# Performance work log

Measured on AMD Instinct MI355X. Metric: run time of the kernel, lower is better.

The kernel has to match this reference:

```python
import jax, jax.numpy as jnp
import numpy as np

CHUNK = 8192
IGNORE_INDEX = -100


def _chunked_logsumexp(hidden, weight, bias, chunk):
    """Online (flash-style) logsumexp over the vocab dim without materializing full logits."""
    V, D = weight.shape
    n_chunks = V // chunk  # V chosen divisible by chunk
    Wc = weight.reshape(n_chunks, chunk, D)
    Bc = bias.reshape(n_chunks, chunk)
    N = hidden.shape[0]

    @jax.checkpoint  # recompute chunk logits in backward, like the original CCE
    def body(carry, wb):
        m, s = carry
        w, b = wb
        logits = hidden @ w.T + b  # [N, chunk]
        cmax = jnp.max(logits, axis=-1)
        new_m = jnp.maximum(m, cmax)
        s = s * jnp.exp(m - new_m) + jnp.sum(jnp.exp(logits - new_m[:, None]), axis=-1)
        return (new_m, s), None

    init = (jnp.full((N,), -jnp.inf, jnp.float32), jnp.zeros((N,), jnp.float32))
    (m, s), _ = jax.lax.scan(body, init, (Wc, Bc))
    return m + jnp.log(s + 1e-10)


def setup_inputs() -> dict:
    key = jax.random.key(0)
    k1, k2, k3, k4 = jax.random.split(key, 4)
    N, D, V = 2048, 1024, 131072
    return {
        "hidden": jax.random.normal(k1, (N, D), dtype=jnp.float32),
        "weight": jax.random.normal(k2, (V, D), dtype=jnp.float32) * 0.02,
        "bias": jax.random.normal(k3, (V,), dtype=jnp.float32) * 0.02,
        "labels": jax.random.randint(k4, (N,), 0, V, dtype=jnp.int32),
    }


def reference(hidden, weight, bias, labels):
    valid = labels != IGNORE_INDEX
    safe_labels = jnp.where(valid, labels, 0)
    lse = _chunked_logsumexp(hidden, weight, bias, CHUNK)  # [N]
    # target logit: only gathers the label rows of weight, never full logits
    target_logit = jnp.einsum("nd,nd->n", hidden, weight[safe_labels]) + bias[safe_labels]
    ce = jnp.where(valid, lse - target_logit, 0.0)
    n_valid = jnp.maximum(jnp.sum(valid), 1).astype(jnp.float32)
    return jnp.sum(ce) / n_valid
```

## Files before the change

kernel.cpp:

```cpp
#include <hip/hip_runtime.h>

#define IGNORE_INDEX (-100)

constexpr int N_ROWS = 2048;
constexpr int D_DIM  = 1024;
constexpr int V_DIM  = 131072;
constexpr int BM = 256, BN = 256, BK = 128;
constexpr int ROW_TILES = N_ROWS / BM;
constexpr int COL_TILES = V_DIM / BN;
constexpr int NBLK = ROW_TILES * COL_TILES;
constexpr int K_TILES = D_DIM / BK;

typedef __attribute__((ext_vector_type(4))) float f32x4;
typedef __attribute__((ext_vector_type(4))) int   i32x4;
typedef __attribute__((ext_vector_type(8))) int   i32x8;

#define SCL_A 0x7F7F7F7Fu
#define SCL_B 0x79797979u

__device__ __forceinline__ unsigned int f2fp4(float f) {
  const float a = fabsf(f);
  unsigned int c = (unsigned)(a >= 0.25f) + (unsigned)(a >= 0.75f) +
                   (unsigned)(a >= 1.25f) + (unsigned)(a >= 1.75f) +
                   (unsigned)(a >= 2.5f)  + (unsigned)(a >= 3.5f) +
                   (unsigned)(a >= 5.0f);
  return c | ((__float_as_uint(f) >> 31) << 3);
}

__global__ __launch_bounds__(256)
void cvt_fp4(const float* __restrict__ src, unsigned char* __restrict__ dst,
             float prescale) {
  const size_t i = ((size_t)blockIdx.x * 256 + (size_t)threadIdx.x) * 32;
  i32x4 o;
#pragma unroll
  for (int q = 0; q < 4; ++q) {
    unsigned int wrd = 0;
#pragma unroll
    for (int e = 0; e < 8; e += 4) {
      const float4 f = *(const float4*)&src[i + q * 8 + e];
      wrd |= f2fp4(f.x * prescale) << ((e + 0) * 4);
      wrd |= f2fp4(f.y * prescale) << ((e + 1) * 4);
      wrd |= f2fp4(f.z * prescale) << ((e + 2) * 4);
      wrd |= f2fp4(f.w * prescale) << ((e + 3) * 4);
    }
    o[q] = (int)wrd;
  }
  *(i32x4*)&dst[i / 2] = o;
}

#define BAR() __builtin_amdgcn_s_barrier()
#define SP1() __builtin_amdgcn_s_setprio(1)
#define SP0() __builtin_amdgcn_s_setprio(0)
#define SCHB() __builtin_amdgcn_sched_barrier(0)
#define VM0() asm volatile("s_waitcnt vmcnt(0)" ::: "memory")

#define STAGE(gbase, ldsoff, kt, buf)                                          \
  {                                                                            \
    _Pragma("unroll") for (int j2_ = 0; j2_ < 2; ++j2_) {                      \
      const char* g_ = (gbase) + (size_t)j2_ * 65536 + (size_t)(kt) * 64;      \
      __builtin_amdgcn_global_load_lds(                                        \
          (const __attribute__((address_space(1))) unsigned int*)g_,           \
          (__attribute__((address_space(3))) unsigned int*)(smem + (ldsoff) +  \
              (buf) * 16384 + j2_ * 8192 + (tid << 4)),                        \
          16, 0, 0);                                                           \
    }                                                                          \
  }

#define READ_FRAG(ldsoff, rowbase, dst)                                        \
  {                                                                            \
    const i32x4 d_ = *(const i32x4*)(smem + (ldsoff) +                         \
                                     ((rowbase) + l15) * 64 + gcol);           \
    dst = (i32x8){d_[0], d_[1], d_[2], d_[3], 0, 0, 0, 0};                     \
  }

__global__ __launch_bounds__(512, 1)
void lse_gemm(const unsigned char* __restrict__ hf4,
              const unsigned char* __restrict__ wf4,
              const float* __restrict__ bias,
              float* __restrict__ ps) {
  __shared__ __align__(16) char smem[69632];

  const int bid = (int)blockIdx.x;
  const int logical = (bid & 7) * (NBLK / 8) + (bid >> 3);
  const int colt = logical >> 3;
  const int m0 = (logical & 7) * BM;
  const int v0 = colt * BN;

  const int tid = threadIdx.x;
  const int w = tid >> 6, lane = tid & 63;
  (void)w;
  const int wm = (tid >> 6) >> 2, wn = (tid >> 6) & 3;
  const int l15 = lane & 15, l16g = lane >> 4;
  const int gcol = (l16g ^ ((l15 >> 1) & 3)) << 4;

  const int r_ = tid >> 2, g_ = tid & 3;
  const int G_ = g_ ^ ((r_ >> 1) & 3);
  const char* habase = (const char*)hf4 + (size_t)(m0 + r_) * 512 + G_ * 16;
  const char* wbase  = (const char*)wf4 + (size_t)(v0 + r_) * 512 + G_ * 16;

  f32x4 acc[8][4];
  const f32x4 zero = {0.f, 0.f, 0.f, 0.f};
#pragma unroll
  for (int i = 0; i < 8; ++i)
#pragma unroll
    for (int j = 0; j < 4; ++j) acc[i][j] = zero;

  i32x8 ar[2], breg[4];

  STAGE(habase, 0, 0, 0);
  STAGE(wbase, 32768, 0, 0);
  SCHB();

#pragma unroll
  for (int t = 0; t < K_TILES; ++t) {
    const int buf = t & 1;
    VM0();
    BAR();
    if (t < K_TILES - 1) {
      STAGE(habase, 0, t + 1, buf ^ 1);
      STAGE(wbase, 32768, t + 1, buf ^ 1);
      SCHB();
    }
#pragma unroll
    for (int q = 0; q < 4; ++q)
      READ_FRAG(32768 + buf * 16384, wn * 64 + q * 16, breg[q]);
    READ_FRAG(buf * 16384, wm * 128, ar[0]);
#pragma unroll
    for (int f = 0; f < 8; ++f) {
      if (f < 7) READ_FRAG(buf * 16384, wm * 128 + (f + 1) * 16, ar[(f + 1) & 1]);
      SP1();
#pragma unroll
      for (int q = 0; q < 4; ++q)
        acc[f][q] = __builtin_amdgcn_mfma_scale_f32_16x16x128_f8f6f4(
            ar[f & 1], breg[q], acc[f][q], 4, 4, 0, SCL_A, 0, SCL_B);
      SP0();
    }
  }
  __syncthreads();

  float* red = (float*)smem;
  float bv[4];
#pragma unroll
  for (int q = 0; q < 4; ++q)
    bv[q] = bias[v0 + wn * 64 + q * 16 + l15];
#pragma unroll
  for (int mi = 0; mi < 8; ++mi) {
#pragma unroll
    for (int r = 0; r < 4; ++r) {
      const float v = __expf(acc[mi][0][r] + bv[0]) + __expf(acc[mi][1][r] + bv[1]) +
                      __expf(acc[mi][2][r] + bv[2]) + __expf(acc[mi][3][r] + bv[3]);
      const int row = wm * 128 + mi * 16 + l16g * 4 + r;
      red[row * 68 + wn * 16 + l15] = v;
    }
  }
  __syncthreads();
  {
    const int row = tid >> 1, h = tid & 1;
    const float* rr = &red[row * 68 + h * 32];
    f32x4 s4 = *(const f32x4*)rr;
#pragma unroll
    for (int i = 1; i < 8; ++i) s4 += *(const f32x4*)(rr + i * 4);
    float s = s4[0] + s4[1] + s4[2] + s4[3];
    s += __shfl_xor(s, 1);
    if (h == 0) ps[(size_t)(m0 + row) * COL_TILES + colt] = s;
  }
}

__global__ __launch_bounds__(256)
void row_finalize(const float* __restrict__ ps,
                  const float* __restrict__ hidden, const float* __restrict__ weight,
                  const float* __restrict__ bias, const int* __restrict__ labels,
                  float* __restrict__ ce) {
  __shared__ float ss[4], sd[4];
  const int row = blockIdx.x;
  const int t = threadIdx.x, lane = t & 63, w = t >> 6;

  float s = 0.f;
#pragma unroll
  for (int i = 0; i < COL_TILES / 256; ++i)
    s += ps[(size_t)row * COL_TILES + t + i * 256];

  const int lbl = labels[row];
  const bool valid = (lbl != IGNORE_INDEX);
  float dot = 0.f;
  if (valid) {
    const float4 h4 = *(const float4*)&hidden[(size_t)row * D_DIM + t * 4];
    const float4 w4 = *(const float4*)&weight[(size_t)lbl * D_DIM + t * 4];
    dot = h4.x * w4.x + h4.y * w4.y + h4.z * w4.z + h4.w * w4.w;
  }
#pragma unroll
  for (int msk = 1; msk < 64; msk <<= 1) {
    s += __shfl_xor(s, msk);
    dot += __shfl_xor(dot, msk);
  }
  if (lane == 0) { ss[w] = s; sd[w] = dot; }
  __syncthreads();
  if (t == 0) {
    const float S = ss[0] + ss[1] + ss[2] + ss[3];
    const float d = sd[0] + sd[1] + sd[2] + sd[3];
    ce[row] = valid ? (logf(S + 1e-10f) - (d + bias[lbl])) : 0.f;
  }
}

__global__ __launch_bounds__(256)
void final_reduce(const float* __restrict__ ce, const int* __restrict__ labels,
                  float* __restrict__ out) {
  __shared__ float ssum[4];
  __shared__ int scnt[4];
  const int t = threadIdx.x, lane = t & 63, w = t >> 6;
  float sum = 0.f; int cnt = 0;
  for (int i = t; i < N_ROWS; i += 256) {
    sum += ce[i];
    cnt += (labels[i] != IGNORE_INDEX) ? 1 : 0;
  }
#pragma unroll
  for (int msk = 1; msk < 64; msk <<= 1) {
    sum += __shfl_xor(sum, msk);
    cnt += __shfl_xor(cnt, msk);
  }
  if (lane == 0) { ssum[w] = sum; scnt[w] = cnt; }
  __syncthreads();
  if (t == 0) {
    const float S = ssum[0] + ssum[1] + ssum[2] + ssum[3];
    const int C = scnt[0] + scnt[1] + scnt[2] + scnt[3];
    out[0] = S / fmaxf((float)C, 1.f);
  }
}

extern "C" void kernel_launch(void* const* d_in, const int* in_sizes, int n_in,
                              void* d_out, int out_size, void* d_ws, size_t ws_size,
                              hipStream_t stream) {
  const float* hidden = (const float*)d_in[0];
  const float* weight = (const float*)d_in[1];
  const float* bias   = (const float*)d_in[2];
  const int*   labels = (const int*)d_in[3];
  float* out = (float*)d_out;

  const size_t WF4_B = (size_t)V_DIM * D_DIM / 2;
  const size_t HF4_B = (size_t)N_ROWS * D_DIM / 2;
  const size_t PS_B  = (size_t)N_ROWS * COL_TILES * 4;
  const size_t CE_B  = (size_t)N_ROWS * 4;
  if (ws_size < WF4_B + HF4_B + PS_B + CE_B) return;

  char* ws = (char*)d_ws;
  unsigned char* wf4 = (unsigned char*)ws;
  unsigned char* hf4 = (unsigned char*)(ws + WF4_B);
  float* ps = (float*)(ws + WF4_B + HF4_B);
  float* ce = (float*)(ws + WF4_B + HF4_B + PS_B);

  cvt_fp4<<<(int)((size_t)V_DIM * D_DIM / 8192), 256, 0, stream>>>(weight, wf4, 64.0f);
  cvt_fp4<<<(int)((size_t)N_ROWS * D_DIM / 8192), 256, 0, stream>>>(hidden, hf4, 1.0f);
  lse_gemm<<<NBLK, 512, 0, stream>>>(hf4, wf4, bias, ps);
  row_finalize<<<N_ROWS, 256, 0, stream>>>(ps, hidden, weight, bias, labels, ce);
  final_reduce<<<1, 256, 0, stream>>>(ce, labels, out);
}
```

Baseline: 312.8 us.

## Pre-shuffle FP4 operands into MFMA fragment order and load directly to registers

The FP4 conversion kernels now write hidden and weight in a fragment-major layout that matches the MFMA operand lanes, so each lane can fetch its 16-byte fragment with one coalesced global load. The GEMM drops the LDS staging, barriers and double buffering, and instead software-pipelines global loads into rotating register buffers (three A fragments, two B sets). This removes LDS traffic and per-tile synchronisation, but it depends on L2/global latency being hidden by register prefetch with only 8 waves per CU, and A fragments are now re-read from global memory by every block rather than shared through LDS.

```diff
diff --git a/kernel.cpp b/kernel.cpp
--- a/kernel.cpp
+++ b/kernel.cpp
@@ -5,11 +5,11 @@
 constexpr int N_ROWS = 2048;
 constexpr int D_DIM  = 1024;
 constexpr int V_DIM  = 131072;
-constexpr int BM = 256, BN = 256, BK = 128;
+constexpr int BM = 256, BN = 256;
 constexpr int ROW_TILES = N_ROWS / BM;
 constexpr int COL_TILES = V_DIM / BN;
 constexpr int NBLK = ROW_TILES * COL_TILES;
-constexpr int K_TILES = D_DIM / BK;
+constexpr int K_TILES = 8;
 
 typedef __attribute__((ext_vector_type(4))) float f32x4;
 typedef __attribute__((ext_vector_type(4))) int   i32x4;
@@ -27,76 +27,58 @@
   return c | ((__float_as_uint(f) >> 31) << 3);
 }
 
+template <int FRAGS>
 __global__ __launch_bounds__(256)
-void cvt_fp4(const float* __restrict__ src, unsigned char* __restrict__ dst,
-             float prescale) {
-  const size_t i = ((size_t)blockIdx.x * 256 + (size_t)threadIdx.x) * 32;
+void cvt_shuf(const float* __restrict__ src, unsigned char* __restrict__ dst,
+              float prescale) {
+  const int oid = blockIdx.x * 256 + threadIdx.x;
+  const int l = oid & 63;
+  int rest = oid >> 6;
+  const int f = rest % FRAGS; rest /= FRAGS;
+  const int t = rest & 7; rest >>= 3;
+  const int row = rest * (FRAGS * 16) + f * 16 + (l & 15);
+  const int col0 = t * 128 + (l >> 4) * 32;
+  const float* s = src + (size_t)row * D_DIM + col0;
   i32x4 o;
 #pragma unroll
-  for (int q = 0; q < 4; ++q) {
-    unsigned int wrd = 0;
+  for (int wd = 0; wd < 4; ++wd) {
+    unsigned int v = 0;
 #pragma unroll
     for (int e = 0; e < 8; e += 4) {
-      const float4 f = *(const float4*)&src[i + q * 8 + e];
-      wrd |= f2fp4(f.x * prescale) << ((e + 0) * 4);
-      wrd |= f2fp4(f.y * prescale) << ((e + 1) * 4);
-      wrd |= f2fp4(f.z * prescale) << ((e + 2) * 4);
-      wrd |= f2fp4(f.w * prescale) << ((e + 3) * 4);
-    }
-    o[q] = (int)wrd;
-  }
-  *(i32x4*)&dst[i / 2] = o;
-}
-
-#define BAR() __builtin_amdgcn_s_barrier()
-#define SP1() __builtin_amdgcn_s_setprio(1)
-#define SP0() __builtin_amdgcn_s_setprio(0)
-#define SCHB() __builtin_amdgcn_sched_barrier(0)
-#define VM0() asm volatile("s_waitcnt vmcnt(0)" ::: "memory")
-
-#define STAGE(gbase, ldsoff, kt, buf)                                          \
-  {                                                                            \
-    _Pragma("unroll") for (int j2_ = 0; j2_ < 2; ++j2_) {                      \
-      const char* g_ = (gbase) + (size_t)j2_ * 65536 + (size_t)(kt) * 64;      \
-      __builtin_amdgcn_global_load_lds(                                        \
-          (const __attribute__((address_space(1))) unsigned int*)g_,           \
-          (__attribute__((address_space(3))) unsigned int*)(smem + (ldsoff) +  \
-              (buf) * 16384 + j2_ * 8192 + (tid << 4)),                        \
-          16, 0, 0);                                                           \
-    }                                                                          \
-  }
-
-#define READ_FRAG(ldsoff, rowbase, dst)                                        \
-  {                                                                            \
-    const i32x4 d_ = *(const i32x4*)(smem + (ldsoff) +                         \
-                                     ((rowbase) + l15) * 64 + gcol);           \
-    dst = (i32x8){d_[0], d_[1], d_[2], d_[3], 0, 0, 0, 0};                     \
-  }
+      const float4 x = *(const float4*)(s + wd * 8 + e);
+      v |= f2fp4(x.x * prescale) << ((e + 0) * 4);
+      v |= f2fp4(x.y * prescale) << ((e + 1) * 4);
+      v |= f2fp4(x.z * prescale) << ((e + 2) * 4);
+      v |= f2fp4(x.w * prescale) << ((e + 3) * 4);
+    }
+    o[wd] = (int)v;
+  }
+  *(i32x4*)(dst + (size_t)oid * 16) = o;
+}
+
+#define LDF(p)                                                                 \
+  ({ const i32x4 d_ = *(const i32x4*)(p);                                      \
+     (i32x8){d_[0], d_[1], d_[2], d_[3], 0, 0, 0, 0}; })
 
 __global__ __launch_bounds__(512, 1)
-void lse_gemm(const unsigned char* __restrict__ hf4,
-              const unsigned char* __restrict__ wf4,
+void lse_gemm(const unsigned char* __restrict__ af4,
+              const unsigned char* __restrict__ bf4,
               const float* __restrict__ bias,
               float* __restrict__ ps) {
-  __shared__ __align__(16) char smem[69632];
+  __shared__ float red[256 * 68];
 
   const int bid = (int)blockIdx.x;
   const int logical = (bid & 7) * (NBLK / 8) + (bid >> 3);
-  const int colt = logical >> 3;
-  const int m0 = (logical & 7) * BM;
-  const int v0 = colt * BN;
-
-  const int tid = threadIdx.x;
-  const int w = tid >> 6, lane = tid & 63;
-  (void)w;
-  const int wm = (tid >> 6) >> 2, wn = (tid >> 6) & 3;
+  const int ct = logical >> 3;
+  const int rt = logical & 7;
+  const int m0 = rt * BM, v0 = ct * BN;
+
+  const int tid = threadIdx.x, lane = tid & 63;
+  const int wid = tid >> 6, wm = wid >> 2, wn = wid & 3;
   const int l15 = lane & 15, l16g = lane >> 4;
-  const int gcol = (l16g ^ ((l15 >> 1) & 3)) << 4;
-
-  const int r_ = tid >> 2, g_ = tid & 3;
-  const int G_ = g_ ^ ((r_ >> 1) & 3);
-  const char* habase = (const char*)hf4 + (size_t)(m0 + r_) * 512 + G_ * 16;
-  const char* wbase  = (const char*)wf4 + (size_t)(v0 + r_) * 512 + G_ * 16;
+
+  const char* ap = (const char*)af4 + ((size_t)(rt * 2 + wm) * 64) * 1024 + lane * 16;
+  const char* bp = (const char*)bf4 + ((size_t)(ct * 4 + wn) * 32) * 1024 + lane * 16;
 
   f32x4 acc[8][4];
   const f32x4 zero = {0.f, 0.f, 0.f, 0.f};
@@ -105,40 +87,31 @@
 #pragma unroll
     for (int j = 0; j < 4; ++j) acc[i][j] = zero;
 
-  i32x8 ar[2], breg[4];
-
-  STAGE(habase, 0, 0, 0);
-  STAGE(wbase, 32768, 0, 0);
-  SCHB();
+  i32x8 ar[3], br[2][4];
+
+#pragma unroll
+  for (int q = 0; q < 4; ++q) br[0][q] = LDF(bp + q * 1024);
+  ar[0] = LDF(ap);
+  ar[1] = LDF(ap + 1024);
 
 #pragma unroll
   for (int t = 0; t < K_TILES; ++t) {
-    const int buf = t & 1;
-    VM0();
-    BAR();
     if (t < K_TILES - 1) {
-      STAGE(habase, 0, t + 1, buf ^ 1);
-      STAGE(wbase, 32768, t + 1, buf ^ 1);
-      SCHB();
-    }
-#pragma unroll
-    for (int q = 0; q < 4; ++q)
-      READ_FRAG(32768 + buf * 16384, wn * 64 + q * 16, breg[q]);
-    READ_FRAG(buf * 16384, wm * 128, ar[0]);
+#pragma unroll
+      for (int q = 0; q < 4; ++q)
+        br[(t + 1) & 1][q] = LDF(bp + (size_t)((t + 1) * 4 + q) * 1024);
+    }
 #pragma unroll
     for (int f = 0; f < 8; ++f) {
-      if (f < 7) READ_FRAG(buf * 16384, wm * 128 + (f + 1) * 16, ar[(f + 1) & 1]);
-      SP1();
+      const int s = t * 8 + f;
+      if (s < 62) ar[(s + 2) % 3] = LDF(ap + (size_t)(s + 2) * 1024);
 #pragma unroll
       for (int q = 0; q < 4; ++q)
         acc[f][q] = __builtin_amdgcn_mfma_scale_f32_16x16x128_f8f6f4(
-            ar[f & 1], breg[q], acc[f][q], 4, 4, 0, SCL_A, 0, SCL_B);
-      SP0();
-    }
-  }
-  __syncthreads();
-
-  float* red = (float*)smem;
+            ar[s % 3], br[t & 1][q], acc[f][q], 4, 4, 0, SCL_A, 0, SCL_B);
+    }
+  }
+
   float bv[4];
 #pragma unroll
   for (int q = 0; q < 4; ++q)
@@ -162,7 +135,7 @@
     for (int i = 1; i < 8; ++i) s4 += *(const f32x4*)(rr + i * 4);
     float s = s4[0] + s4[1] + s4[2] + s4[3];
     s += __shfl_xor(s, 1);
-    if (h == 0) ps[(size_t)(m0 + row) * COL_TILES + colt] = s;
+    if (h == 0) ps[(size_t)(m0 + row) * COL_TILES + ct] = s;
   }
 }
 
@@ -237,20 +210,20 @@
   float* out = (float*)d_out;
 
   const size_t WF4_B = (size_t)V_DIM * D_DIM / 2;
-  const size_t HF4_B = (size_t)N_ROWS * D_DIM / 2;
+  const size_t AF4_B = (size_t)N_ROWS * D_DIM / 2;
   const size_t PS_B  = (size_t)N_ROWS * COL_TILES * 4;
   const size_t CE_B  = (size_t)N_ROWS * 4;
-  if (ws_size < WF4_B + HF4_B + PS_B + CE_B) return;
+  if (ws_size < WF4_B + AF4_B + PS_B + CE_B) return;
 
   char* ws = (char*)d_ws;
   unsigned char* wf4 = (unsigned char*)ws;
-  unsigned char* hf4 = (unsigned char*)(ws + WF4_B);
-  float* ps = (float*)(ws + WF4_B + HF4_B);
-  float* ce = (float*)(ws + WF4_B + HF4_B + PS_B);
-
-  cvt_fp4<<<(int)((size_t)V_DIM * D_DIM / 8192), 256, 0, stream>>>(weight, wf4, 64.0f);
-  cvt_fp4<<<(int)((size_t)N_ROWS * D_DIM / 8192), 256, 0, stream>>>(hidden, hf4, 1.0f);
-  lse_gemm<<<NBLK, 512, 0, stream>>>(hf4, wf4, bias, ps);
+  unsigned char* af4 = (unsigned char*)(ws + WF4_B);
+  float* ps = (float*)(ws + WF4_B + AF4_B);
+  float* ce = (float*)(ws + WF4_B + AF4_B + PS_B);
+
+  cvt_shuf<4><<<16384, 256, 0, stream>>>(weight, wf4, 64.0f);
+  cvt_shuf<8><<<256, 256, 0, stream>>>(hidden, af4, 1.0f);
+  lse_gemm<<<NBLK, 512, 0, stream>>>(af4, wf4, bias, ps);
   row_finalize<<<N_ROWS, 256, 0, stream>>>(ps, hidden, weight, bias, labels, ce);
   final_reduce<<<1, 256, 0, stream>>>(ce, labels, out);
 }
```

Measured after the change: 435.9 us. 1.39x slower.

## Fuse weight FP4 conversion into GEMM with LDS-resident weight tiles

Applied to the files above, without the earlier changes.

Drops the separate pass that converts the whole weight matrix to FP4 in global memory. Each of 256 blocks now owns four 128-column vocab tiles and keeps the FP4 weight tile resident in LDS, double buffered. While it loops over all row tiles of the hidden states, it converts the next weight tile from fp32, interleaved with the MFMA work. This removes the global write and re-read of the FP4 weights. In exchange each block streams the hidden FP4 data once per vocab tile, uses more LDS, and the grid is only 256 blocks.

```diff
diff --git a/kernel.cpp b/kernel.cpp
--- a/kernel.cpp
+++ b/kernel.cpp
@@ -5,11 +5,11 @@
 constexpr int N_ROWS = 2048;
 constexpr int D_DIM  = 1024;
 constexpr int V_DIM  = 131072;
-constexpr int BM = 256, BN = 256, BK = 128;
+constexpr int BM = 256, BN = 128, BK = 128;
 constexpr int ROW_TILES = N_ROWS / BM;
 constexpr int COL_TILES = V_DIM / BN;
-constexpr int NBLK = ROW_TILES * COL_TILES;
 constexpr int K_TILES = D_DIM / BK;
+constexpr int PPB = 4;
 
 typedef __attribute__((ext_vector_type(4))) float f32x4;
 typedef __attribute__((ext_vector_type(4))) int   i32x4;
@@ -28,8 +28,7 @@
 }
 
 __global__ __launch_bounds__(256)
-void cvt_fp4(const float* __restrict__ src, unsigned char* __restrict__ dst,
-             float prescale) {
+void cvt_fp4(const float* __restrict__ src, unsigned char* __restrict__ dst) {
   const size_t i = ((size_t)blockIdx.x * 256 + (size_t)threadIdx.x) * 32;
   i32x4 o;
 #pragma unroll
@@ -38,10 +37,10 @@
 #pragma unroll
     for (int e = 0; e < 8; e += 4) {
       const float4 f = *(const float4*)&src[i + q * 8 + e];
-      wrd |= f2fp4(f.x * prescale) << ((e + 0) * 4);
-      wrd |= f2fp4(f.y * prescale) << ((e + 1) * 4);
-      wrd |= f2fp4(f.z * prescale) << ((e + 2) * 4);
-      wrd |= f2fp4(f.w * prescale) << ((e + 3) * 4);
+      wrd |= f2fp4(f.x) << ((e + 0) * 4);
+      wrd |= f2fp4(f.y) << ((e + 1) * 4);
+      wrd |= f2fp4(f.z) << ((e + 2) * 4);
+      wrd |= f2fp4(f.w) << ((e + 3) * 4);
     }
     o[q] = (int)wrd;
   }
@@ -54,115 +53,142 @@
 #define SCHB() __builtin_amdgcn_sched_barrier(0)
 #define VM0() asm volatile("s_waitcnt vmcnt(0)" ::: "memory")
 
-#define STAGE(gbase, ldsoff, kt, buf)                                          \
+#define STAGE_A(rtoff, kt, ab)                                                 \
   {                                                                            \
     _Pragma("unroll") for (int j2_ = 0; j2_ < 2; ++j2_) {                      \
-      const char* g_ = (gbase) + (size_t)j2_ * 65536 + (size_t)(kt) * 64;      \
+      const char* g_ = hab + (rtoff) + (size_t)j2_ * 65536 + (size_t)(kt) * 64;\
       __builtin_amdgcn_global_load_lds(                                        \
           (const __attribute__((address_space(1))) unsigned int*)g_,           \
-          (__attribute__((address_space(3))) unsigned int*)(smem + (ldsoff) +  \
-              (buf) * 16384 + j2_ * 8192 + (tid << 4)),                        \
+          (__attribute__((address_space(3))) unsigned int*)(smem + 131072 +    \
+              (ab) * 16384 + j2_ * 8192 + (tid << 4)),                         \
           16, 0, 0);                                                           \
     }                                                                          \
   }
 
-#define READ_FRAG(ldsoff, rowbase, dst)                                        \
+#define READ_FRAG(base, rowbase, dst)                                          \
   {                                                                            \
-    const i32x4 d_ = *(const i32x4*)(smem + (ldsoff) +                         \
+    const i32x4 d_ = *(const i32x4*)(smem + (base) +                           \
                                      ((rowbase) + l15) * 64 + gcol);           \
     dst = (i32x8){d_[0], d_[1], d_[2], d_[3], 0, 0, 0, 0};                     \
   }
 
 __global__ __launch_bounds__(512, 1)
-void lse_gemm(const unsigned char* __restrict__ hf4,
-              const unsigned char* __restrict__ wf4,
-              const float* __restrict__ bias,
-              float* __restrict__ ps) {
-  __shared__ __align__(16) char smem[69632];
-
-  const int bid = (int)blockIdx.x;
-  const int logical = (bid & 7) * (NBLK / 8) + (bid >> 3);
-  const int colt = logical >> 3;
-  const int m0 = (logical & 7) * BM;
-  const int v0 = colt * BN;
+void lse_fused(const unsigned char* __restrict__ hf4,
+               const float* __restrict__ weight,
+               const float* __restrict__ bias,
+               float* __restrict__ ps) {
+  __shared__ __align__(16) char smem[163840];
 
   const int tid = threadIdx.x;
-  const int w = tid >> 6, lane = tid & 63;
-  (void)w;
-  const int wm = (tid >> 6) >> 2, wn = (tid >> 6) & 3;
+  const int lane = tid & 63;
+  const int wv = tid >> 6, wm = wv >> 1, wn = wv & 1;
   const int l15 = lane & 15, l16g = lane >> 4;
   const int gcol = (l16g ^ ((l15 >> 1) & 3)) << 4;
 
-  const int r_ = tid >> 2, g_ = tid & 3;
-  const int G_ = g_ ^ ((r_ >> 1) & 3);
-  const char* habase = (const char*)hf4 + (size_t)(m0 + r_) * 512 + G_ * 16;
-  const char* wbase  = (const char*)wf4 + (size_t)(v0 + r_) * 512 + G_ * 16;
-
-  f32x4 acc[8][4];
+  const int ra_ = tid >> 2;
+  const int Ga_ = (tid & 3) ^ ((ra_ >> 1) & 3);
+  const char* hab = (const char*)hf4 + (size_t)ra_ * 512 + Ga_ * 16;
+
+  const int sub = tid & 7, Gc = (tid >> 3) & 3, ktc = (tid >> 5) & 7;
+  const int rhi = tid >> 8;
+  const int cvsrc = ktc * 128 + Gc * 32 + sub * 4;
+
+  f32x4 acc[4][4];
   const f32x4 zero = {0.f, 0.f, 0.f, 0.f};
-#pragma unroll
-  for (int i = 0; i < 8; ++i)
-#pragma unroll
-    for (int j = 0; j < 4; ++j) acc[i][j] = zero;
-
   i32x8 ar[2], breg[4];
 
-  STAGE(habase, 0, 0, 0);
-  STAGE(wbase, 32768, 0, 0);
-  SCHB();
-
-#pragma unroll
-  for (int t = 0; t < K_TILES; ++t) {
-    const int buf = t & 1;
-    VM0();
-    BAR();
-    if (t < K_TILES - 1) {
-      STAGE(habase, 0, t + 1, buf ^ 1);
-      STAGE(wbase, 32768, t + 1, buf ^ 1);
-      SCHB();
+  {
+    const int v00 = blockIdx.x * PPB * BN;
+#pragma unroll 4
+    for (int i = 0; i < 64; ++i) {
+      const int rr = 2 * i + rhi;
+      const float4 wx = *(const float4*)&weight[(size_t)(v00 + rr) * 1024 + cvsrc];
+      const unsigned int b0 = f2fp4(wx.x * 64.f) | (f2fp4(wx.y * 64.f) << 4);
+      const unsigned int b1 = f2fp4(wx.z * 64.f) | (f2fp4(wx.w * 64.f) << 4);
+      *(unsigned short*)(smem + ktc * 8192 + rr * 64 + ((Gc ^ (i & 3)) << 4) +
+                         sub * 2) = (unsigned short)(b0 | (b1 << 8));
     }
+  }
+  __syncthreads();
+
+  int cur = 0;
+  for (int p = 0; p < PPB; ++p) {
+    const int colt = blockIdx.x * PPB + p;
+    const int v0 = colt * BN;
+    const int v0n = v0 + BN;
+    const bool docvt = (p < PPB - 1);
+    const int nxt = cur ^ 1;
+
+    float bv[4];
 #pragma unroll
     for (int q = 0; q < 4; ++q)
-      READ_FRAG(32768 + buf * 16384, wn * 64 + q * 16, breg[q]);
-    READ_FRAG(buf * 16384, wm * 128, ar[0]);
-#pragma unroll
-    for (int f = 0; f < 8; ++f) {
-      if (f < 7) READ_FRAG(buf * 16384, wm * 128 + (f + 1) * 16, ar[(f + 1) & 1]);
-      SP1();
-#pragma unroll
-      for (int q = 0; q < 4; ++q)
-        acc[f][q] = __builtin_amdgcn_mfma_scale_f32_16x16x128_f8f6f4(
-            ar[f & 1], breg[q], acc[f][q], 4, 4, 0, SCL_A, 0, SCL_B);
-      SP0();
+      bv[q] = bias[v0 + wn * 64 + q * 16 + l15];
+
+    for (int rt = 0; rt < ROW_TILES; ++rt) {
+      const size_t rtoff = (size_t)rt * 131072;
+#pragma unroll
+      for (int i = 0; i < 4; ++i)
+#pragma unroll
+        for (int j = 0; j < 4; ++j) acc[i][j] = zero;
+
+      STAGE_A(rtoff, 0, 0);
+#pragma unroll
+      for (int kt = 0; kt < K_TILES; ++kt) {
+        VM0();
+        BAR();
+        SCHB();
+        const int i = rt * 8 + kt;
+        const int rr = 2 * i + rhi;
+        float4 wx;
+        if (docvt)
+          wx = *(const float4*)&weight[(size_t)(v0n + rr) * 1024 + cvsrc];
+        if (kt < K_TILES - 1) STAGE_A(rtoff, kt + 1, (kt + 1) & 1);
+        SCHB();
+#pragma unroll
+        for (int q = 0; q < 4; ++q)
+          READ_FRAG(cur * 65536 + kt * 8192, wn * 64 + q * 16, breg[q]);
+        READ_FRAG(131072 + (kt & 1) * 16384, wm * 64, ar[0]);
+#pragma unroll
+        for (int f = 0; f < 4; ++f) {
+          if (f < 3)
+            READ_FRAG(131072 + (kt & 1) * 16384, wm * 64 + (f + 1) * 16,
+                      ar[(f + 1) & 1]);
+          SP1();
+#pragma unroll
+          for (int q = 0; q < 4; ++q)
+            acc[f][q] = __builtin_amdgcn_mfma_scale_f32_16x16x128_f8f6f4(
+                ar[f & 1], breg[q], acc[f][q], 4, 4, 0, SCL_A, 0, SCL_B);
+          SP0();
+        }
+        if (docvt) {
+          const unsigned int b0 = f2fp4(wx.x * 64.f) | (f2fp4(wx.y * 64.f) << 4);
+          const unsigned int b1 = f2fp4(wx.z * 64.f) | (f2fp4(wx.w * 64.f) << 4);
+          *(unsigned short*)(smem + nxt * 65536 + ktc * 8192 + rr * 64 +
+                             ((Gc ^ (i & 3)) << 4) + sub * 2) =
+              (unsigned short)(b0 | (b1 << 8));
+        }
+      }
+      __syncthreads();
+      float* red = (float*)(smem + 131072);
+#pragma unroll
+      for (int mi = 0; mi < 4; ++mi) {
+#pragma unroll
+        for (int r = 0; r < 4; ++r) {
+          float se = __expf(acc[mi][0][r] + bv[0]) + __expf(acc[mi][1][r] + bv[1]) +
+                     __expf(acc[mi][2][r] + bv[2]) + __expf(acc[mi][3][r] + bv[3]);
+          se += __shfl_xor(se, 8); se += __shfl_xor(se, 4);
+          se += __shfl_xor(se, 2); se += __shfl_xor(se, 1);
+          if (l15 == 0)
+            red[(wm * 64 + mi * 16 + l16g * 4 + r) * 2 + wn] = se;
+        }
+      }
+      __syncthreads();
+      if (tid < BM)
+        ps[(size_t)(rt * BM + tid) * COL_TILES + colt] =
+            red[tid * 2] + red[tid * 2 + 1];
+      __syncthreads();
     }
-  }
-  __syncthreads();
-
-  float* red = (float*)smem;
-  float bv[4];
-#pragma unroll
-  for (int q = 0; q < 4; ++q)
-    bv[q] = bias[v0 + wn * 64 + q * 16 + l15];
-#pragma unroll
-  for (int mi = 0; mi < 8; ++mi) {
-#pragma unroll
-    for (int r = 0; r < 4; ++r) {
-      const float v = __expf(acc[mi][0][r] + bv[0]) + __expf(acc[mi][1][r] + bv[1]) +
-                      __expf(acc[mi][2][r] + bv[2]) + __expf(acc[mi][3][r] + bv[3]);
-      const int row = wm * 128 + mi * 16 + l16g * 4 + r;
-      red[row * 68 + wn * 16 + l15] = v;
-    }
-  }
-  __syncthreads();
-  {
-    const int row = tid >> 1, h = tid & 1;
-    const float* rr = &red[row * 68 + h * 32];
-    f32x4 s4 = *(const f32x4*)rr;
-#pragma unroll
-    for (int i = 1; i < 8; ++i) s4 += *(const f32x4*)(rr + i * 4);
-    float s = s4[0] + s4[1] + s4[2] + s4[3];
-    s += __shfl_xor(s, 1);
-    if (h == 0) ps[(size_t)(m0 + row) * COL_TILES + colt] = s;
+    cur ^= 1;
   }
 }
 
@@ -236,21 +262,18 @@
   const int*   labels = (const int*)d_in[3];
   float* out = (float*)d_out;
 
-  const size_t WF4_B = (size_t)V_DIM * D_DIM / 2;
   const size_t HF4_B = (size_t)N_ROWS * D_DIM / 2;
   const size_t PS_B  = (size_t)N_ROWS * COL_TILES * 4;
   const size_t CE_B  = (size_t)N_ROWS * 4;
-  if (ws_size < WF4_B + HF4_B + PS_B + CE_B) return;
+  if (ws_size < HF4_B + PS_B + CE_B) return;
 
   char* ws = (char*)d_ws;
-  unsigned char* wf4 = (unsigned char*)ws;
-  unsigned char* hf4 = (unsigned char*)(ws + WF4_B);
-  float* ps = (float*)(ws + WF4_B + HF4_B);
-  float* ce = (float*)(ws + WF4_B + HF4_B + PS_B);
-
-  cvt_fp4<<<(int)((size_t)V_DIM * D_DIM / 8192), 256, 0, stream>>>(weight, wf4, 64.0f);
-  cvt_fp4<<<(int)((size_t)N_ROWS * D_DIM / 8192), 256, 0, stream>>>(hidden, hf4, 1.0f);
-  lse_gemm<<<NBLK, 512, 0, stream>>>(hf4, wf4, bias, ps);
+  unsigned char* hf4 = (unsigned char*)ws;
+  float* ps = (float*)(ws + HF4_B);
+  float* ce = (float*)(ws + HF4_B + PS_B);
+
+  cvt_fp4<<<(int)((size_t)N_ROWS * D_DIM / 8192), 256, 0, stream>>>(hidden, hf4);
+  lse_fused<<<256, 512, 0, stream>>>(hf4, weight, bias, ps);
   row_finalize<<<N_ROWS, 256, 0, stream>>>(ps, hidden, weight, bias, labels, ce);
   final_reduce<<<1, 256, 0, stream>>>(ce, labels, out);
 }
```

After: 770.2 us. 2.46x slower.
